# Kernel tuning notes

Hardware: AMD Instinct MI355X
Metric: run time of the kernel (lower is better)

The kernel has to match this reference:

```python
import jax, jax.numpy as jnp
import numpy as np

B, T, D, H = 1024, 200, 128, 128


def setup_inputs() -> dict:
    key = jax.random.key(0)
    k1, k2, k3, k4 = jax.random.split(key, 4)
    item_his_eb = jax.random.normal(k1, (B, T, D), dtype=jnp.float32)
    seq_len = jax.random.randint(k2, (B,), 0, T, dtype=jnp.int32)
    # TF GRUCell packs [r, u] gates in one matmul over concat([x, h]).
    W_gate = jax.random.normal(k3, (D + H, 2 * H), dtype=jnp.float32) * (1.0 / np.sqrt(D + H))
    b_gate = jnp.ones((2 * H,), dtype=jnp.float32)  # TF GRUCell bias init = 1.0
    W_cand = jax.random.normal(k4, (D + H, H), dtype=jnp.float32) * (1.0 / np.sqrt(D + H))
    b_cand = jnp.zeros((H,), dtype=jnp.float32)
    return {"item_his_eb": item_his_eb, "seq_len": seq_len,
            "W_gate": W_gate, "b_gate": b_gate,
            "W_cand": W_cand, "b_cand": b_cand}


def reference(item_his_eb, seq_len, W_gate, b_gate, W_cand, b_cand):
    # dynamic_rnn(GRUCell(H)) with sequence_length masking.
    # Outputs are zero and state is held for steps t >= seq_len.
    Bq, Tq, Dq = item_his_eb.shape
    Hq = W_cand.shape[1]
    x_tbd = jnp.transpose(item_his_eb, (1, 0, 2))  # [T, B, D]

    def step(h, inp):
        x_t, t = inp  # x_t: [B, D], t: scalar int
        gates = jax.nn.sigmoid(jnp.concatenate([x_t, h], axis=-1) @ W_gate + b_gate)
        r, u = jnp.split(gates, 2, axis=-1)  # each [B, H]
        c = jnp.tanh(jnp.concatenate([x_t, r * h], axis=-1) @ W_cand + b_cand)
        h_new = u * h + (1.0 - u) * c
        valid = (t < seq_len)[:, None]  # [B, 1]
        h_next = jnp.where(valid, h_new, h)
        y = jnp.where(valid, h_new, jnp.zeros_like(h_new))
        return h_next, y

    h0 = jnp.zeros((Bq, Hq), dtype=item_his_eb.dtype)
    _, ys = jax.lax.scan(step, h0, (x_tbd, jnp.arange(Tq)))
    return jnp.transpose(ys, (1, 0, 2))  # [B, T, H]
```

## Files before the change

### kernel.cpp

```cpp
#include <hip/hip_runtime.h>

#define T_SZ 200
#define H_SZ 128

typedef __attribute__((ext_vector_type(8))) short    bf16x8;
typedef __attribute__((ext_vector_type(4))) float    f32x4;
typedef __attribute__((ext_vector_type(4))) int      i32x4;
typedef __attribute__((ext_vector_type(2))) unsigned u32x2;

__device__ __forceinline__ unsigned short f2bf(float f) {
  unsigned u = __builtin_bit_cast(unsigned, f);
  u += 0x7fffu + ((u >> 16) & 1u);
  return (unsigned short)(u >> 16);
}
__device__ __forceinline__ unsigned cvt_pk_bf16(float a, float b) {
  unsigned r;
  asm("v_cvt_pk_bf16_f32 %0, %1, %2" : "=v"(r) : "v"(a), "v"(b));
  return r;
}
__device__ __forceinline__ float sigmoid_fast(float x) {
  float e = __builtin_amdgcn_exp2f(-1.442695041f * x);
  return __builtin_amdgcn_rcpf(1.0f + e);
}
__device__ __forceinline__ float tanh_fast(float x) {
  float e = __builtin_amdgcn_exp2f(2.885390082f * x);
  return 1.0f - 2.0f * __builtin_amdgcn_rcpf(e + 1.0f);
}
__device__ __forceinline__ void ldsbar() {
  __asm__ __volatile__("" ::: "memory");
  __builtin_amdgcn_s_waitcnt(0xc07f);
  __builtin_amdgcn_s_barrier();
  __asm__ __volatile__("" ::: "memory");
}

__global__ __launch_bounds__(512, 1) void gru_fused(
    const float* __restrict__ X,
    const int*   __restrict__ seq_len,
    const float* __restrict__ Wg,
    const float* __restrict__ bg,
    const float* __restrict__ Wc,
    const float* __restrict__ bc,
    float* __restrict__ Y)
{
  __shared__ unsigned short hA[16 * 136];
  __shared__ unsigned short rhA[16 * 136];
  __shared__ unsigned short xA[2][16 * 136];

  const int tid  = threadIdx.x;
  const int lane = tid & 63;
  const int w    = tid >> 6;
  const int m16  = lane & 15;
  const int q    = lane >> 4;

  bf16x8 wgf[2][8];
  #pragma unroll
  for (int nt = 0; nt < 2; ++nt) {
    int col = nt * 128 + w * 16 + m16;
    #pragma unroll
    for (int kb = 0; kb < 8; ++kb) {
      bf16x8 f;
      #pragma unroll
      for (int j = 0; j < 8; ++j)
        f[j] = (short)f2bf(Wg[(size_t)(kb * 32 + q * 8 + j) * 256 + col]);
      wgf[nt][kb] = f;
    }
  }
  const int colc = w * 16 + m16;
  bf16x8 wcf[8];
  #pragma unroll
  for (int kb = 0; kb < 8; ++kb) {
    bf16x8 f;
    #pragma unroll
    for (int j = 0; j < 8; ++j)
      f[j] = (short)f2bf(Wc[(size_t)(kb * 32 + q * 8 + j) * 128 + colc]);
    wcf[kb] = f;
  }

  const int col4 = w * 16 + q * 4;
  const f32x4 gbias_r = *(const f32x4*)&bg[col4];
  const f32x4 gbias_u = *(const f32x4*)&bg[128 + col4];
  const f32x4 cbias4  = *(const f32x4*)&bc[col4];

  const int bt = blockIdx.x;
  const int slen = seq_len[bt * 16 + m16];

  float h[4] = {0.f, 0.f, 0.f, 0.f};

  for (int idx = tid; idx < 16 * 136; idx += 512) hA[idx] = 0;

  const int xrow = tid >> 5;
  const int xk4  = (tid & 31) * 4;
  const float* xbase = X + (size_t)(bt * 16 + xrow) * T_SZ * 128 + xk4;

  auto xload = [&](int t, f32x4& r) {
    r = *(const f32x4*)(xbase + (size_t)t * 128);
  };
  auto xstage = [&](int buf, const f32x4& r) {
    unsigned d0 = cvt_pk_bf16(r.x, r.y);
    unsigned d1 = cvt_pk_bf16(r.z, r.w);
    *(u32x2*)&xA[buf][xrow * 136 + xk4] = (u32x2){d0, d1};
  };

  f32x4 x0r, x1r, xrE, xrO;
  xload(0, x0r); xload(1, x1r);
  xstage(0, x0r); xstage(1, x1r);
  xload(2, xrE); xload(3, xrO);
  ldsbar();

  f32x4 axrA, axuA, ccA, axrB, axuB, ccB;
  {
    bf16x8 xaf[4];
    #pragma unroll
    for (int kb = 0; kb < 4; ++kb)
      xaf[kb] = __builtin_bit_cast(bf16x8, *(const i32x4*)&xA[0][m16 * 136 + kb * 32 + q * 8]);
    f32x4 cc = cbias4, ar = gbias_r, au = gbias_u;
    #pragma unroll
    for (int kb = 0; kb < 4; ++kb) {
      cc = __builtin_amdgcn_mfma_f32_16x16x32_bf16(wcf[kb],    xaf[kb], cc, 0, 0, 0);
      ar = __builtin_amdgcn_mfma_f32_16x16x32_bf16(wgf[0][kb], xaf[kb], ar, 0, 0, 0);
      au = __builtin_amdgcn_mfma_f32_16x16x32_bf16(wgf[1][kb], xaf[kb], au, 0, 0, 0);
    }
    ccA = cc; axrA = ar; axuA = au;
  }
  ldsbar();

  float* const ybase = Y + (size_t)(bt * 16 + m16) * T_SZ * H_SZ + col4;

  auto step = [&](int t, f32x4& xreg,
                  f32x4& axin_r, f32x4& axin_u, f32x4& ccin,
                  f32x4& axout_r, f32x4& axout_u, f32x4& ccout) {
    bf16x8 haf[4];
    #pragma unroll
    for (int kb = 0; kb < 4; ++kb)
      haf[kb] = __builtin_bit_cast(bf16x8, *(const i32x4*)&hA[m16 * 136 + kb * 32 + q * 8]);

    if (t < 198) xstage(t & 1, xreg);
    if (t < 196) xload(t + 4, xreg);

    f32x4 ra = axin_r, rb = { 0.f, 0.f, 0.f, 0.f };
    ra = __builtin_amdgcn_mfma_f32_16x16x32_bf16(wgf[0][4], haf[0], ra, 0, 0, 0);
    ra = __builtin_amdgcn_mfma_f32_16x16x32_bf16(wgf[0][5], haf[1], ra, 0, 0, 0);
    rb = __builtin_amdgcn_mfma_f32_16x16x32_bf16(wgf[0][6], haf[2], rb, 0, 0, 0);
    rb = __builtin_amdgcn_mfma_f32_16x16x32_bf16(wgf[0][7], haf[3], rb, 0, 0, 0);

    float rh0 = sigmoid_fast(ra[0] + rb[0]) * h[0];
    float rh1 = sigmoid_fast(ra[1] + rb[1]) * h[1];
    float rh2 = sigmoid_fast(ra[2] + rb[2]) * h[2];
    float rh3 = sigmoid_fast(ra[3] + rb[3]) * h[3];
    *(u32x2*)&rhA[m16 * 136 + col4] =
        (u32x2){ cvt_pk_bf16(rh0, rh1), cvt_pk_bf16(rh2, rh3) };
    ldsbar();

    bf16x8 rhf[4];
    #pragma unroll
    for (int kb = 0; kb < 4; ++kb)
      rhf[kb] = __builtin_bit_cast(bf16x8, *(const i32x4*)&rhA[m16 * 136 + kb * 32 + q * 8]);
    bf16x8 xaf2[4];
    if (t < 199) {
      const unsigned short* xb = xA[(t + 1) & 1];
      #pragma unroll
      for (int kb = 0; kb < 4; ++kb)
        xaf2[kb] = __builtin_bit_cast(bf16x8, *(const i32x4*)&xb[m16 * 136 + kb * 32 + q * 8]);
    }

    f32x4 ua = axin_u;
    ua = __builtin_amdgcn_mfma_f32_16x16x32_bf16(wgf[1][4], haf[0], ua, 0, 0, 0);
    ua = __builtin_amdgcn_mfma_f32_16x16x32_bf16(wgf[1][5], haf[1], ua, 0, 0, 0);
    ua = __builtin_amdgcn_mfma_f32_16x16x32_bf16(wgf[1][6], haf[2], ua, 0, 0, 0);
    ua = __builtin_amdgcn_mfma_f32_16x16x32_bf16(wgf[1][7], haf[3], ua, 0, 0, 0);

    f32x4 ca = ccin, cb = { 0.f, 0.f, 0.f, 0.f };
    ca = __builtin_amdgcn_mfma_f32_16x16x32_bf16(wcf[4], rhf[0], ca, 0, 0, 0);
    ca = __builtin_amdgcn_mfma_f32_16x16x32_bf16(wcf[5], rhf[1], ca, 0, 0, 0);
    cb = __builtin_amdgcn_mfma_f32_16x16x32_bf16(wcf[6], rhf[2], cb, 0, 0, 0);
    cb = __builtin_amdgcn_mfma_f32_16x16x32_bf16(wcf[7], rhf[3], cb, 0, 0, 0);

    if (t < 199) {
      f32x4 cc = cbias4, ar = gbias_r, au = gbias_u;
      #pragma unroll
      for (int kb = 0; kb < 4; ++kb) {
        cc = __builtin_amdgcn_mfma_f32_16x16x32_bf16(wcf[kb],    xaf2[kb], cc, 0, 0, 0);
        ar = __builtin_amdgcn_mfma_f32_16x16x32_bf16(wgf[0][kb], xaf2[kb], ar, 0, 0, 0);
        au = __builtin_amdgcn_mfma_f32_16x16x32_bf16(wgf[1][kb], xaf2[kb], au, 0, 0, 0);
      }
      ccout = cc; axout_r = ar; axout_u = au;
    }

    const bool valid = (t < slen);
    f32x4 yv;
    #pragma unroll
    for (int i = 0; i < 4; ++i) {
      float u  = sigmoid_fast(ua[i]);
      float c  = tanh_fast(ca[i] + cb[i]);
      float hn = u * (h[i] - c) + c;
      h[i]  = valid ? hn : h[i];
      yv[i] = valid ? hn : 0.0f;
    }
    *(f32x4*)(ybase + (size_t)t * H_SZ) = yv;
    *(u32x2*)&hA[m16 * 136 + col4] =
        (u32x2){ cvt_pk_bf16(h[0], h[1]), cvt_pk_bf16(h[2], h[3]) };
    ldsbar();
  };

  for (int t = 0; t < 200; t += 2) {
    step(t,     xrE, axrA, axuA, ccA, axrB, axuB, ccB);
    step(t + 1, xrO, axrB, axuB, ccB, axrA, axuA, ccA);
  }
}

extern "C" void kernel_launch(void* const* d_in, const int* in_sizes, int n_in,
                              void* d_out, int out_size, void* d_ws, size_t ws_size,
                              hipStream_t stream) {
  const float* X   = (const float*)d_in[0];
  const int*   seq = (const int*)  d_in[1];
  const float* Wg  = (const float*)d_in[2];
  const float* bg  = (const float*)d_in[3];
  const float* Wc  = (const float*)d_in[4];
  const float* bc  = (const float*)d_in[5];
  float* Y = (float*)d_out;
  (void)d_ws; (void)ws_size;

  hipLaunchKernelGGL(gru_fused, dim3(64), dim3(512), 0, stream,
                     X, seq, Wg, bg, Wc, bc, Y);
}
```

Before: 324.4 us.

## Halve block to 4 waves, each computing two 16-column tiles per step

Shrinks the block from 8 waves to 4, so each wave owns two 16-column output tiles of the hidden state and holds twice the weight fragments in registers. Pairs of independent MFMA chains are interleaved to hide MFMA latency, and the per-step LDS barriers now synchronise fewer waves. The trade-off is more register pressure (about 48 bf16x8 weight fragments per lane, with a risk of spills) and more serial MFMA work per wave on the recurrent critical path.

```diff
diff --git a/kernel.cpp b/kernel.cpp
--- a/kernel.cpp
+++ b/kernel.cpp
@@ -33,7 +33,9 @@
   __asm__ __volatile__("" ::: "memory");
 }
 
-__global__ __launch_bounds__(512, 1) void gru_fused(
+#define MFMA __builtin_amdgcn_mfma_f32_16x16x32_bf16
+
+__global__ __launch_bounds__(256, 1) void gru_fused(
     const float* __restrict__ X,
     const int*   __restrict__ seq_len,
     const float* __restrict__ Wg,
@@ -52,103 +54,115 @@
   const int m16  = lane & 15;
   const int q    = lane >> 4;
 
-  bf16x8 wgf[2][8];
+  bf16x8 wr[2][8], wu[2][8], wc[2][8];
   #pragma unroll
-  for (int nt = 0; nt < 2; ++nt) {
-    int col = nt * 128 + w * 16 + m16;
+  for (int t2 = 0; t2 < 2; ++t2) {
+    const int colr = (2 * w + t2) * 16 + m16;
     #pragma unroll
     for (int kb = 0; kb < 8; ++kb) {
-      bf16x8 f;
-      #pragma unroll
-      for (int j = 0; j < 8; ++j)
-        f[j] = (short)f2bf(Wg[(size_t)(kb * 32 + q * 8 + j) * 256 + col]);
-      wgf[nt][kb] = f;
-    }
-  }
-  const int colc = w * 16 + m16;
-  bf16x8 wcf[8];
+      bf16x8 fr, fu, fc;
+      #pragma unroll
+      for (int j = 0; j < 8; ++j) {
+        const int k = kb * 32 + q * 8 + j;
+        fr[j] = (short)f2bf(Wg[(size_t)k * 256 + colr]);
+        fu[j] = (short)f2bf(Wg[(size_t)k * 256 + 128 + colr]);
+        fc[j] = (short)f2bf(Wc[(size_t)k * 128 + colr]);
+      }
+      wr[t2][kb] = fr; wu[t2][kb] = fu; wc[t2][kb] = fc;
+    }
+  }
+  f32x4 br4[2], bu4[2], bcc4[2];
   #pragma unroll
-  for (int kb = 0; kb < 8; ++kb) {
-    bf16x8 f;
-    #pragma unroll
-    for (int j = 0; j < 8; ++j)
-      f[j] = (short)f2bf(Wc[(size_t)(kb * 32 + q * 8 + j) * 128 + colc]);
-    wcf[kb] = f;
-  }
-
-  const int col4 = w * 16 + q * 4;
-  const f32x4 gbias_r = *(const f32x4*)&bg[col4];
-  const f32x4 gbias_u = *(const f32x4*)&bg[128 + col4];
-  const f32x4 cbias4  = *(const f32x4*)&bc[col4];
-
-  const int bt = blockIdx.x;
+  for (int t2 = 0; t2 < 2; ++t2) {
+    const int c4 = (2 * w + t2) * 16 + q * 4;
+    br4[t2]  = *(const f32x4*)&bg[c4];
+    bu4[t2]  = *(const f32x4*)&bg[128 + c4];
+    bcc4[t2] = *(const f32x4*)&bc[c4];
+  }
+
+  const int bt   = blockIdx.x;
   const int slen = seq_len[bt * 16 + m16];
 
-  float h[4] = {0.f, 0.f, 0.f, 0.f};
-
-  for (int idx = tid; idx < 16 * 136; idx += 512) hA[idx] = 0;
-
-  const int xrow = tid >> 5;
-  const int xk4  = (tid & 31) * 4;
-  const float* xbase = X + (size_t)(bt * 16 + xrow) * T_SZ * 128 + xk4;
-
-  auto xload = [&](int t, f32x4& r) {
-    r = *(const f32x4*)(xbase + (size_t)t * 128);
+  float h0[4] = {0.f, 0.f, 0.f, 0.f};
+  float h1[4] = {0.f, 0.f, 0.f, 0.f};
+
+  for (int idx = tid; idx < 16 * 136; idx += 256) hA[idx] = 0;
+
+  const int xrow = tid >> 4;
+  const int xk8  = (tid & 15) * 8;
+  const float* xbase = X + (size_t)(bt * 16 + xrow) * T_SZ * 128 + xk8;
+
+  auto xload = [&](int t, f32x4& a, f32x4& b) {
+    const float* p = xbase + (size_t)t * 128;
+    a = *(const f32x4*)p;
+    b = *(const f32x4*)(p + 4);
   };
-  auto xstage = [&](int buf, const f32x4& r) {
-    unsigned d0 = cvt_pk_bf16(r.x, r.y);
-    unsigned d1 = cvt_pk_bf16(r.z, r.w);
-    *(u32x2*)&xA[buf][xrow * 136 + xk4] = (u32x2){d0, d1};
+  auto xstage = [&](int buf, const f32x4& a, const f32x4& b) {
+    i32x4 pk = { (int)cvt_pk_bf16(a.x, a.y), (int)cvt_pk_bf16(a.z, a.w),
+                 (int)cvt_pk_bf16(b.x, b.y), (int)cvt_pk_bf16(b.z, b.w) };
+    *(i32x4*)&xA[buf][xrow * 136 + xk8] = pk;
   };
 
-  f32x4 x0r, x1r, xrE, xrO;
-  xload(0, x0r); xload(1, x1r);
-  xstage(0, x0r); xstage(1, x1r);
-  xload(2, xrE); xload(3, xrO);
+  f32x4 t0a, t0b, t1a, t1b, xrEa, xrEb, xrOa, xrOb;
+  xload(0, t0a, t0b); xload(1, t1a, t1b);
+  xstage(0, t0a, t0b); xstage(1, t1a, t1b);
+  xload(2, xrEa, xrEb); xload(3, xrOa, xrOb);
   ldsbar();
 
-  f32x4 axrA, axuA, ccA, axrB, axuB, ccB;
+  f32x4 axr[2], axu[2], ccp[2];
   {
     bf16x8 xaf[4];
     #pragma unroll
     for (int kb = 0; kb < 4; ++kb)
       xaf[kb] = __builtin_bit_cast(bf16x8, *(const i32x4*)&xA[0][m16 * 136 + kb * 32 + q * 8]);
-    f32x4 cc = cbias4, ar = gbias_r, au = gbias_u;
-    #pragma unroll
-    for (int kb = 0; kb < 4; ++kb) {
-      cc = __builtin_amdgcn_mfma_f32_16x16x32_bf16(wcf[kb],    xaf[kb], cc, 0, 0, 0);
-      ar = __builtin_amdgcn_mfma_f32_16x16x32_bf16(wgf[0][kb], xaf[kb], ar, 0, 0, 0);
-      au = __builtin_amdgcn_mfma_f32_16x16x32_bf16(wgf[1][kb], xaf[kb], au, 0, 0, 0);
-    }
-    ccA = cc; axrA = ar; axuA = au;
+    #pragma unroll
+    for (int t2 = 0; t2 < 2; ++t2) {
+      f32x4 c_ = bcc4[t2], r_ = br4[t2], u_ = bu4[t2];
+      #pragma unroll
+      for (int kb = 0; kb < 4; ++kb) {
+        c_ = MFMA(wc[t2][kb], xaf[kb], c_, 0, 0, 0);
+        r_ = MFMA(wr[t2][kb], xaf[kb], r_, 0, 0, 0);
+        u_ = MFMA(wu[t2][kb], xaf[kb], u_, 0, 0, 0);
+      }
+      ccp[t2] = c_; axr[t2] = r_; axu[t2] = u_;
+    }
   }
   ldsbar();
 
-  float* const ybase = Y + (size_t)(bt * 16 + m16) * T_SZ * H_SZ + col4;
-
-  auto step = [&](int t, f32x4& xreg,
-                  f32x4& axin_r, f32x4& axin_u, f32x4& ccin,
-                  f32x4& axout_r, f32x4& axout_u, f32x4& ccout) {
+  float* const yb0 = Y + (size_t)(bt * 16 + m16) * T_SZ * H_SZ + 2 * w * 16 + q * 4;
+  const int lw0 = m16 * 136 + 2 * w * 16 + q * 4;
+  const int lw1 = lw0 + 16;
+
+  auto step = [&](int t, f32x4& xra, f32x4& xrb) {
     bf16x8 haf[4];
     #pragma unroll
     for (int kb = 0; kb < 4; ++kb)
       haf[kb] = __builtin_bit_cast(bf16x8, *(const i32x4*)&hA[m16 * 136 + kb * 32 + q * 8]);
 
-    if (t < 198) xstage(t & 1, xreg);
-    if (t < 196) xload(t + 4, xreg);
-
-    f32x4 ra = axin_r, rb = { 0.f, 0.f, 0.f, 0.f };
-    ra = __builtin_amdgcn_mfma_f32_16x16x32_bf16(wgf[0][4], haf[0], ra, 0, 0, 0);
-    ra = __builtin_amdgcn_mfma_f32_16x16x32_bf16(wgf[0][5], haf[1], ra, 0, 0, 0);
-    rb = __builtin_amdgcn_mfma_f32_16x16x32_bf16(wgf[0][6], haf[2], rb, 0, 0, 0);
-    rb = __builtin_amdgcn_mfma_f32_16x16x32_bf16(wgf[0][7], haf[3], rb, 0, 0, 0);
-
-    float rh0 = sigmoid_fast(ra[0] + rb[0]) * h[0];
-    float rh1 = sigmoid_fast(ra[1] + rb[1]) * h[1];
-    float rh2 = sigmoid_fast(ra[2] + rb[2]) * h[2];
-    float rh3 = sigmoid_fast(ra[3] + rb[3]) * h[3];
-    *(u32x2*)&rhA[m16 * 136 + col4] =
-        (u32x2){ cvt_pk_bf16(rh0, rh1), cvt_pk_bf16(rh2, rh3) };
+    if (t < 198) xstage(t & 1, xra, xrb);
+    if (t < 196) xload(t + 4, xra, xrb);
+
+    f32x4 r0a = axr[0], r0b = {0.f,0.f,0.f,0.f};
+    f32x4 r1a = axr[1], r1b = {0.f,0.f,0.f,0.f};
+    r0a = MFMA(wr[0][4], haf[0], r0a, 0, 0, 0);
+    r1a = MFMA(wr[1][4], haf[0], r1a, 0, 0, 0);
+    r0a = MFMA(wr[0][5], haf[1], r0a, 0, 0, 0);
+    r1a = MFMA(wr[1][5], haf[1], r1a, 0, 0, 0);
+    r0b = MFMA(wr[0][6], haf[2], r0b, 0, 0, 0);
+    r1b = MFMA(wr[1][6], haf[2], r1b, 0, 0, 0);
+    r0b = MFMA(wr[0][7], haf[3], r0b, 0, 0, 0);
+    r1b = MFMA(wr[1][7], haf[3], r1b, 0, 0, 0);
+
+    float s00 = sigmoid_fast(r0a[0] + r0b[0]) * h0[0];
+    float s01 = sigmoid_fast(r0a[1] + r0b[1]) * h0[1];
+    float s02 = sigmoid_fast(r0a[2] + r0b[2]) * h0[2];
+    float s03 = sigmoid_fast(r0a[3] + r0b[3]) * h0[3];
+    float s10 = sigmoid_fast(r1a[0] + r1b[0]) * h1[0];
+    float s11 = sigmoid_fast(r1a[1] + r1b[1]) * h1[1];
+    float s12 = sigmoid_fast(r1a[2] + r1b[2]) * h1[2];
+    float s13 = sigmoid_fast(r1a[3] + r1b[3]) * h1[3];
+    *(u32x2*)&rhA[lw0] = (u32x2){ cvt_pk_bf16(s00, s01), cvt_pk_bf16(s02, s03) };
+    *(u32x2*)&rhA[lw1] = (u32x2){ cvt_pk_bf16(s10, s11), cvt_pk_bf16(s12, s13) };
     ldsbar();
 
     bf16x8 rhf[4];
@@ -163,48 +177,69 @@
         xaf2[kb] = __builtin_bit_cast(bf16x8, *(const i32x4*)&xb[m16 * 136 + kb * 32 + q * 8]);
     }
 
-    f32x4 ua = axin_u;
-    ua = __builtin_amdgcn_mfma_f32_16x16x32_bf16(wgf[1][4], haf[0], ua, 0, 0, 0);
-    ua = __builtin_amdgcn_mfma_f32_16x16x32_bf16(wgf[1][5], haf[1], ua, 0, 0, 0);
-    ua = __builtin_amdgcn_mfma_f32_16x16x32_bf16(wgf[1][6], haf[2], ua, 0, 0, 0);
-    ua = __builtin_amdgcn_mfma_f32_16x16x32_bf16(wgf[1][7], haf[3], ua, 0, 0, 0);
-
-    f32x4 ca = ccin, cb = { 0.f, 0.f, 0.f, 0.f };
-    ca = __builtin_amdgcn_mfma_f32_16x16x32_bf16(wcf[4], rhf[0], ca, 0, 0, 0);
-    ca = __builtin_amdgcn_mfma_f32_16x16x32_bf16(wcf[5], rhf[1], ca, 0, 0, 0);
-    cb = __builtin_amdgcn_mfma_f32_16x16x32_bf16(wcf[6], rhf[2], cb, 0, 0, 0);
-    cb = __builtin_amdgcn_mfma_f32_16x16x32_bf16(wcf[7], rhf[3], cb, 0, 0, 0);
+    f32x4 u0 = axu[0], u1 = axu[1];
+    u0 = MFMA(wu[0][4], haf[0], u0, 0, 0, 0);
+    u1 = MFMA(wu[1][4], haf[0], u1, 0, 0, 0);
+    u0 = MFMA(wu[0][5], haf[1], u0, 0, 0, 0);
+    u1 = MFMA(wu[1][5], haf[1], u1, 0, 0, 0);
+    u0 = MFMA(wu[0][6], haf[2], u0, 0, 0, 0);
+    u1 = MFMA(wu[1][6], haf[2], u1, 0, 0, 0);
+    u0 = MFMA(wu[0][7], haf[3], u0, 0, 0, 0);
+    u1 = MFMA(wu[1][7], haf[3], u1, 0, 0, 0);
+
+    f32x4 c0a = ccp[0], c0b = {0.f,0.f,0.f,0.f};
+    f32x4 c1a = ccp[1], c1b = {0.f,0.f,0.f,0.f};
+    c0a = MFMA(wc[0][4], rhf[0], c0a, 0, 0, 0);
+    c1a = MFMA(wc[1][4], rhf[0], c1a, 0, 0, 0);
+    c0a = MFMA(wc[0][5], rhf[1], c0a, 0, 0, 0);
+    c1a = MFMA(wc[1][5], rhf[1], c1a, 0, 0, 0);
+    c0b = MFMA(wc[0][6], rhf[2], c0b, 0, 0, 0);
+    c1b = MFMA(wc[1][6], rhf[2], c1b, 0, 0, 0);
+    c0b = MFMA(wc[0][7], rhf[3], c0b, 0, 0, 0);
+    c1b = MFMA(wc[1][7], rhf[3], c1b, 0, 0, 0);
 
     if (t < 199) {
-      f32x4 cc = cbias4, ar = gbias_r, au = gbias_u;
-      #pragma unroll
-      for (int kb = 0; kb < 4; ++kb) {
-        cc = __builtin_amdgcn_mfma_f32_16x16x32_bf16(wcf[kb],    xaf2[kb], cc, 0, 0, 0);
-        ar = __builtin_amdgcn_mfma_f32_16x16x32_bf16(wgf[0][kb], xaf2[kb], ar, 0, 0, 0);
-        au = __builtin_amdgcn_mfma_f32_16x16x32_bf16(wgf[1][kb], xaf2[kb], au, 0, 0, 0);
+      #pragma unroll
+      for (int t2 = 0; t2 < 2; ++t2) {
+        f32x4 c_ = bcc4[t2], r_ = br4[t2], u_ = bu4[t2];
+        #pragma unroll
+        for (int kb = 0; kb < 4; ++kb) {
+          c_ = MFMA(wc[t2][kb], xaf2[kb], c_, 0, 0, 0);
+          r_ = MFMA(wr[t2][kb], xaf2[kb], r_, 0, 0, 0);
+          u_ = MFMA(wu[t2][kb], xaf2[kb], u_, 0, 0, 0);
+        }
+        ccp[t2] = c_; axr[t2] = r_; axu[t2] = u_;
       }
-      ccout = cc; axout_r = ar; axout_u = au;
     }
 
     const bool valid = (t < slen);
-    f32x4 yv;
+    f32x4 y0, y1;
     #pragma unroll
     for (int i = 0; i < 4; ++i) {
-      float u  = sigmoid_fast(ua[i]);
-      float c  = tanh_fast(ca[i] + cb[i]);
-      float hn = u * (h[i] - c) + c;
-      h[i]  = valid ? hn : h[i];
-      yv[i] = valid ? hn : 0.0f;
-    }
-    *(f32x4*)(ybase + (size_t)t * H_SZ) = yv;
-    *(u32x2*)&hA[m16 * 136 + col4] =
-        (u32x2){ cvt_pk_bf16(h[0], h[1]), cvt_pk_bf16(h[2], h[3]) };
+      float uu = sigmoid_fast(u0[i]);
+      float cc = tanh_fast(c0a[i] + c0b[i]);
+      float hn = uu * (h0[i] - cc) + cc;
+      h0[i] = valid ? hn : h0[i];
+      y0[i] = valid ? hn : 0.0f;
+    }
+    #pragma unroll
+    for (int i = 0; i < 4; ++i) {
+      float uu = sigmoid_fast(u1[i]);
+      float cc = tanh_fast(c1a[i] + c1b[i]);
+      float hn = uu * (h1[i] - cc) + cc;
+      h1[i] = valid ? hn : h1[i];
+      y1[i] = valid ? hn : 0.0f;
+    }
+    *(f32x4*)(yb0 + (size_t)t * H_SZ)      = y0;
+    *(f32x4*)(yb0 + (size_t)t * H_SZ + 16) = y1;
+    *(u32x2*)&hA[lw0] = (u32x2){ cvt_pk_bf16(h0[0], h0[1]), cvt_pk_bf16(h0[2], h0[3]) };
+    *(u32x2*)&hA[lw1] = (u32x2){ cvt_pk_bf16(h1[0], h1[1]), cvt_pk_bf16(h1[2], h1[3]) };
     ldsbar();
   };
 
   for (int t = 0; t < 200; t += 2) {
-    step(t,     xrE, axrA, axuA, ccA, axrB, axuB, ccB);
-    step(t + 1, xrO, axrB, axuB, ccB, axrA, axuA, ccA);
+    step(t,     xrEa, xrEb);
+    step(t + 1, xrOa, xrOb);
   }
 }
 
@@ -220,6 +255,6 @@
   float* Y = (float*)d_out;
   (void)d_ws; (void)ws_size;
 
-  hipLaunchKernelGGL(gru_fused, dim3(64), dim3(512), 0, stream,
+  hipLaunchKernelGGL(gru_fused, dim3(64), dim3(256), 0, stream,
                      X, seq, Wg, bg, Wc, bc, Y);
 }
```

Measured after the change: 380.2 us. +17.2%, slower.
